# Performance work log

Measured on AMD Instinct MI355X. Metric: run time of the kernel, lower is better.

The kernel has to match this reference:

```python
import jax, jax.numpy as jnp
import numpy as np

B, T, D = 256, 256, 128   # batch, timesteps, latent_dims
U1 = 512                  # units for gru1/gru2
U3 = 64                   # n_output for gru3


def _glorot(key, shape):
    fan_in, fan_out = shape[0], shape[1]
    lim = np.sqrt(6.0 / (fan_in + fan_out))
    return jax.random.uniform(key, shape, jnp.float32, -lim, lim)


def setup_inputs() -> dict:
    key = jax.random.key(0)
    ks = jax.random.split(key, 10)
    inp = {"x": jax.random.normal(ks[0], (B, T, D), jnp.float32)}
    # Keras GRU (reset_after=True): kernel [in, 3u], recurrent_kernel [u, 3u], bias [2, 3u]
    inp["W1"] = _glorot(ks[1], (D, 3 * U1))
    inp["R1"] = _glorot(ks[2], (U1, 3 * U1))
    inp["b1"] = jnp.zeros((2, 3 * U1), jnp.float32)
    inp["W2"] = _glorot(ks[3], (U1, 3 * U1))
    inp["R2"] = _glorot(ks[4], (U1, 3 * U1))
    inp["b2"] = jnp.zeros((2, 3 * U1), jnp.float32)
    inp["W3"] = _glorot(ks[5], (U1, 3 * U3))
    inp["R3"] = _glorot(ks[6], (U3, 3 * U3))
    inp["b3"] = jnp.zeros((2, 3 * U3), jnp.float32)
    return inp


def gru_layer(x, W, R, b, act):
    """Keras GRU, reset_after=True, recurrent_activation=sigmoid, gate order z,r,h.
    x: [B,T,Din] -> [B,T,u] (return_sequences=True)."""
    u = R.shape[0]
    # precompute input projection for all timesteps: [B,T,3u]
    xproj = jnp.einsum('btd,dk->btk', x, W) + b[0]

    def step(h, xt):
        rec = h @ R + b[1]                      # [B,3u]
        xz, xr, xh = jnp.split(xt, 3, axis=-1)
        rz, rr, rh = jnp.split(rec, 3, axis=-1)
        z = jax.nn.sigmoid(xz + rz)
        r = jax.nn.sigmoid(xr + rr)
        hh = act(xh + r * rh)                   # reset gate applied after recurrent matmul
        h_new = z * h + (1.0 - z) * hh
        return h_new, h_new

    h0 = jnp.zeros((x.shape[0], u), x.dtype)
    _, ys = jax.lax.scan(step, h0, jnp.swapaxes(xproj, 0, 1))  # scan over time
    return jnp.swapaxes(ys, 0, 1)


def reference(x, W1, R1, b1, W2, R2, b2, W3, R3, b3):
    h = gru_layer(x, W1, R1, b1, jax.nn.relu)
    h = gru_layer(h, W2, R2, b2, jax.nn.relu)   # dropout skipped (training=False)
    return gru_layer(h, W3, R3, b3, jax.nn.sigmoid)
```

## Files before the change

### kernel.cpp

```cpp
#include <hip/hip_runtime.h>

typedef unsigned short ushort_t;
typedef unsigned int uint_t;
typedef unsigned long long ull_t;
typedef __attribute__((ext_vector_type(8))) short short8;
typedef __attribute__((ext_vector_type(4))) float f32x4;

#define MFMA16(a, b, c) __builtin_amdgcn_mfma_f32_16x16x32_bf16((a), (b), (c), 0, 0, 0)

__device__ __forceinline__ ushort_t f2bf(float f) {
  union { float f; uint_t u; } v; v.f = f;
  uint_t r = v.u + 0x7fffu + ((v.u >> 16) & 1u);
  return (ushort_t)(r >> 16);
}
__device__ __forceinline__ float sigm(float x) { return 1.f / (1.f + __expf(-x)); }

__device__ __forceinline__ short8 ldc(const ushort_t* p) {
  union { ull_t q[2]; short8 v; } u;
  u.q[0] = __hip_atomic_load((const ull_t*)p, __ATOMIC_RELAXED, __HIP_MEMORY_SCOPE_AGENT);
  u.q[1] = __hip_atomic_load((const ull_t*)(p + 4), __ATOMIC_RELAXED, __HIP_MEMORY_SCOPE_AGENT);
  return u.v;
}
template <bool SEQ>
__device__ __forceinline__ short8 ldh(const ushort_t* p) {
  if constexpr (SEQ) return *(const short8*)p;
  else return ldc(p);
}
__device__ __forceinline__ void stc8(ushort_t* p, ull_t v) {
  __hip_atomic_store((ull_t*)p, v, __ATOMIC_RELAXED, __HIP_MEMORY_SCOPE_AGENT);
}
__device__ __forceinline__ void stc4(uint_t* p, uint_t v) {
  __hip_atomic_store(p, v, __ATOMIC_RELAXED, __HIP_MEMORY_SCOPE_AGENT);
}

__device__ __forceinline__ void barrier_l() {
  asm volatile("s_waitcnt lgkmcnt(0)" ::: "memory");
  __builtin_amdgcn_s_barrier();
  asm volatile("" ::: "memory");
}

__device__ __forceinline__ size_t hidx(int ko, int b0, int l15) {
  return (size_t)((ko >> 4) * 256 + b0 + l15) * 16 + (ko & 15);
}

#define OFF_XBF  0UL
#define OFF_W1T  16777216UL
#define OFF_R1T  17170432UL
#define OFF_W2T  18743296UL
#define OFF_R2T  20316160UL
#define OFF_W3T  21889024UL
#define OFF_R3T  22085632UL
#define OFF_CNT  22110208UL
#define OFF_H    22114304UL
#define H1_BYTES_SEQ  (257UL * 262144UL)
#define H3_BYTES_SEQ  (257UL * 32768UL)
#define SEQ_NEED (OFF_H + 2UL * H1_BYTES_SEQ + H3_BYTES_SEQ)
#define H1_BYTES_RING (4UL * 262144UL)

__global__ void k_cvtx(const float* __restrict__ x, ushort_t* __restrict__ xb) {
  const int i = blockIdx.x * 256 + threadIdx.x;
  const int d4 = i & 31;
  const int t = (i >> 5) & 255;
  const int b = i >> 13;
  const float4 v = ((const float4*)x)[i];
  ushort4 o;
  o.x = f2bf(v.x); o.y = f2bf(v.y); o.z = f2bf(v.z); o.w = f2bf(v.w);
  ((ushort4*)xb)[(((t << 8) + b) << 5) + d4] = o;
}

__global__ void k_tr(const float* __restrict__ src, ushort_t* __restrict__ dst,
                     int K, int G, int n) {
  const int i = blockIdx.x * 256 + threadIdx.x;
  if (i >= n) return;
  const int g = i / K, k = i - g * K;
  dst[i] = f2bf(src[(size_t)k * G + g]);
}

__global__ void k_zero(uint_t* h1, uint_t* h2, uint_t* h3, uint_t* cnt) {
  const int i = blockIdx.x * 256 + threadIdx.x;
  if (i < 65536) h1[i] = 0;
  else if (i < 131072) h2[i - 65536] = 0;
  else if (i < 139264) h3[i - 131072] = 0;
  else if (i < 139776) cnt[i - 139264] = 0;
}

template <bool SEQ>
__global__ __launch_bounds__(256, 1)
void gru_main(const ushort_t* __restrict__ xbf,
              const ushort_t* __restrict__ W1t, const ushort_t* __restrict__ R1t,
              const ushort_t* __restrict__ W2t, const ushort_t* __restrict__ R2t,
              const ushort_t* __restrict__ W3t, const ushort_t* __restrict__ R3t,
              const float* __restrict__ b1, const float* __restrict__ b2,
              const float* __restrict__ b3,
              ushort_t* __restrict__ h1s, ushort_t* __restrict__ h2s,
              ushort_t* __restrict__ h3s,
              uint_t* __restrict__ cnt, float* __restrict__ out) {
  __shared__ char ldsb[64512] __attribute__((aligned(16)));
  char* w2b = ldsb + 15360;
#define RGN(r) (*(f32x4*)(ldsb + ((r) << 10) + ((size_t)lane << 4)))
  const int tid = threadIdx.x, bid = blockIdx.x;
  const int grp = bid & 7;
  const int w = bid >> 3;
  const int b0A = grp << 5, b0B = b0A + 16;
  const int lane = tid & 63, wid = tid >> 6;
  const int l15 = lane & 15, quad = lane >> 4, q8 = quad << 3;
  const int lay = wid >> 1, sub = wid & 1;
  const bool isC = (w >= 28);
  const int u = (w << 4) + l15;
  const int u3 = ((w - 28) << 4) + l15;

  if (lay == 1) {
#pragma unroll
    for (int g = 0; g < 3; ++g)
#pragma unroll
      for (int kk = 0; kk < 8; ++kk) {
        const int k2 = sub * 8 + kk;
        const short8 v = *(const short8*)&W2t[(size_t)(g * 512 + u) * 512 + k2 * 32 + q8];
        const int off = ((((g * 16 + l15) << 10) + ((k2 * 32 + q8) << 1)) ^ ((l15 & 7) << 4));
        *(short8*)(w2b + off) = v;
      }
  }

  short8 wreg[33];
  if (lay == 0) {
    if (sub == 0) {
#pragma unroll
      for (int g = 0; g < 3; ++g) {
#pragma unroll
        for (int kk = 0; kk < 4; ++kk)
          wreg[g * 4 + kk] = *(const short8*)&W1t[(size_t)(g * 512 + u) * 128 + kk * 32 + q8];
#pragma unroll
        for (int kk = 0; kk < 5; ++kk)
          wreg[12 + g * 5 + kk] = *(const short8*)&R1t[(size_t)(g * 512 + u) * 512 + kk * 32 + q8];
      }
    } else {
#pragma unroll
      for (int g = 0; g < 3; ++g)
#pragma unroll
        for (int kk = 0; kk < 11; ++kk)
          wreg[g * 11 + kk] = *(const short8*)&R1t[(size_t)(g * 512 + u) * 512 + (5 + kk) * 32 + q8];
    }
  } else {
#pragma unroll
    for (int g = 0; g < 3; ++g)
#pragma unroll
      for (int kk = 0; kk < 8; ++kk)
        wreg[g * 8 + kk] = *(const short8*)&R2t[(size_t)(g * 512 + u) * 512 + (sub * 8 + kk) * 32 + q8];
  }
  __syncthreads();

  const float bzs1 = b1[u] + b1[1536 + u];
  const float brs1 = b1[512 + u] + b1[2048 + u];
  const float bh10 = b1[1024 + u], bh11 = b1[2560 + u];
  const float bzs2 = b2[u] + b2[1536 + u];
  const float brs2 = b2[512 + u] + b2[2048 + u];
  const float bh20 = b2[1024 + u], bh21 = b2[2560 + u];
  float czs = 0, crs = 0, ch0 = 0, ch1 = 0;
  if (isC) {
    czs = b3[u3] + b3[192 + u3];
    crs = b3[64 + u3] + b3[256 + u3];
    ch0 = b3[128 + u3]; ch1 = b3[320 + u3];
  }

  float h1st[4] = {0, 0, 0, 0};
  float h2st[4] = {0, 0, 0, 0};
  float h3st[4] = {0, 0, 0, 0};
  const f32x4 z4 = {0.f, 0.f, 0.f, 0.f};
  uint_t* flags = cnt;

#pragma unroll 1
  for (int s = 0; s < 258; ++s) {
    {
      const uint_t* fl = flags + grp * 32 + (lane & 31);
      while (true) {
        const uint_t v = __hip_atomic_load(fl, __ATOMIC_RELAXED, __HIP_MEMORY_SCOPE_AGENT);
        if (__all((int)(v >= (uint_t)s))) break;
        __builtin_amdgcn_s_sleep(1);
      }
      asm volatile("" ::: "memory");
    }
    const size_t sl_h1rd = (size_t)(SEQ ? s : (s & 3)) * 131072;
    const size_t sl_h1wr = (size_t)(SEQ ? (s + 1) : ((s + 1) & 3)) * 131072;
    const size_t sl_h2rd = (size_t)(SEQ ? (s - 1) : ((s - 1) & 3)) * 131072;
    const size_t sl_h2wr = (size_t)(SEQ ? s : (s & 3)) * 131072;
    const size_t sl_h3rd = (size_t)(SEQ ? (s - 2) : ((s - 2) & 3)) * 16384;
    const size_t sl_h3wr = (size_t)(SEQ ? (s - 1) : ((s - 1) & 3)) * 16384;

    f32x4 azA = z4, arrA = z4, ahxA = z4, ahrA = z4;
    f32x4 azB = z4, arrB = z4, ahxB = z4, ahrB = z4;
    f32x4 dzA = z4, drrA = z4, dhxA = z4, dhrA = z4;
    f32x4 dzB = z4, drrB = z4, dhxB = z4, dhrB = z4;

    if (lay == 0) {
      const ushort_t* h1rd = h1s + sl_h1rd;
      const ushort_t* h2rd = h2s + sl_h2rd;
      if (sub == 0) {
        short8 sx[4], sh[5], s2A[8], s3[2];
        if (s < 256) {
          const ushort_t* xrA = xbf + ((size_t)s * 256 + b0A + l15) * 128;
#pragma unroll
          for (int kk = 0; kk < 4; ++kk) sx[kk] = *(const short8*)&xrA[kk * 32 + q8];
#pragma unroll
          for (int kk = 0; kk < 5; ++kk)
            sh[kk] = ldh<SEQ>(&h1rd[hidx(kk * 32 + q8, b0A, l15)]);
        }
        if (isC && s >= 2) {
          const ushort_t* h3rd = h3s + sl_h3rd;
#pragma unroll
          for (int kk = 0; kk < 8; ++kk)
            s2A[kk] = ldh<SEQ>(&h2rd[hidx(kk * 32 + q8, b0A, l15)]);
#pragma unroll
          for (int kk = 0; kk < 2; ++kk)
            s3[kk] = ldh<SEQ>(&h3rd[hidx(kk * 32 + q8, b0A, l15)]);
        }
        if (s < 256) {
#pragma unroll
          for (int kk = 0; kk < 4; ++kk) {
            azA  = MFMA16(sx[kk], wreg[kk], azA);
            arrA = MFMA16(sx[kk], wreg[4 + kk], arrA);
            ahxA = MFMA16(sx[kk], wreg[8 + kk], ahxA);
          }
#pragma unroll
          for (int kk = 0; kk < 5; ++kk) {
            azA  = MFMA16(sh[kk], wreg[12 + kk], azA);
            arrA = MFMA16(sh[kk], wreg[17 + kk], arrA);
            ahrA = MFMA16(sh[kk], wreg[22 + kk], ahrA);
          }
          const ushort_t* xrB = xbf + ((size_t)s * 256 + b0B + l15) * 128;
#pragma unroll
          for (int kk = 0; kk < 4; ++kk) sx[kk] = *(const short8*)&xrB[kk * 32 + q8];
#pragma unroll
          for (int kk = 0; kk < 5; ++kk)
            sh[kk] = ldh<SEQ>(&h1rd[hidx(kk * 32 + q8, b0B, l15)]);
#pragma unroll
          for (int kk = 0; kk < 4; ++kk) {
            azB  = MFMA16(sx[kk], wreg[kk], azB);
            arrB = MFMA16(sx[kk], wreg[4 + kk], arrB);
            ahxB = MFMA16(sx[kk], wreg[8 + kk], ahxB);
          }
#pragma unroll
          for (int kk = 0; kk < 5; ++kk) {
            azB  = MFMA16(sh[kk], wreg[12 + kk], azB);
            arrB = MFMA16(sh[kk], wreg[17 + kk], arrB);
            ahrB = MFMA16(sh[kk], wreg[22 + kk], ahrB);
          }
        }
        if (isC && s >= 2) {
          const ushort_t* h3rd = h3s + sl_h3rd;
#pragma unroll
          for (int kk = 0; kk < 8; ++kk) {
            const int ko = kk * 32 + q8;
            dzA  = MFMA16(s2A[kk], *(const short8*)&W3t[(size_t)u3 * 512 + ko], dzA);
            drrA = MFMA16(s2A[kk], *(const short8*)&W3t[(size_t)(64 + u3) * 512 + ko], drrA);
            dhxA = MFMA16(s2A[kk], *(const short8*)&W3t[(size_t)(128 + u3) * 512 + ko], dhxA);
          }
#pragma unroll
          for (int kk = 0; kk < 2; ++kk) {
            const int ko = kk * 32 + q8;
            dzA  = MFMA16(s3[kk], *(const short8*)&R3t[(size_t)u3 * 64 + ko], dzA);
            drrA = MFMA16(s3[kk], *(const short8*)&R3t[(size_t)(64 + u3) * 64 + ko], drrA);
            dhrA = MFMA16(s3[kk], *(const short8*)&R3t[(size_t)(128 + u3) * 64 + ko], dhrA);
          }
#pragma unroll
          for (int kk = 0; kk < 8; ++kk)
            s2A[kk] = ldh<SEQ>(&h2rd[hidx(kk * 32 + q8, b0B, l15)]);
#pragma unroll
          for (int kk = 0; kk < 2; ++kk)
            s3[kk] = ldh<SEQ>(&h3rd[hidx(kk * 32 + q8, b0B, l15)]);
#pragma unroll
          for (int kk = 0; kk < 8; ++kk) {
            const int ko = kk * 32 + q8;
            dzB  = MFMA16(s2A[kk], *(const short8*)&W3t[(size_t)u3 * 512 + ko], dzB);
            drrB = MFMA16(s2A[kk], *(const short8*)&W3t[(size_t)(64 + u3) * 512 + ko], drrB);
            dhxB = MFMA16(s2A[kk], *(const short8*)&W3t[(size_t)(128 + u3) * 512 + ko], dhxB);
          }
#pragma unroll
          for (int kk = 0; kk < 2; ++kk) {
            const int ko = kk * 32 + q8;
            dzB  = MFMA16(s3[kk], *(const short8*)&R3t[(size_t)u3 * 64 + ko], dzB);
            drrB = MFMA16(s3[kk], *(const short8*)&R3t[(size_t)(64 + u3) * 64 + ko], drrB);
            dhrB = MFMA16(s3[kk], *(const short8*)&R3t[(size_t)(128 + u3) * 64 + ko], dhrB);
          }
        }
      } else {
        short8 sh[11], s2A[8];
        if (s < 256) {
#pragma unroll
          for (int kk = 0; kk < 11; ++kk)
            sh[kk] = ldh<SEQ>(&h1rd[hidx((5 + kk) * 32 + q8, b0A, l15)]);
        }
        if (isC && s >= 2) {
#pragma unroll
          for (int kk = 0; kk < 8; ++kk)
            s2A[kk] = ldh<SEQ>(&h2rd[hidx((8 + kk) * 32 + q8, b0A, l15)]);
        }
        if (s < 256) {
#pragma unroll
          for (int kk = 0; kk < 11; ++kk) {
            azA  = MFMA16(sh[kk], wreg[kk], azA);
            arrA = MFMA16(sh[kk], wreg[11 + kk], arrA);
            ahrA = MFMA16(sh[kk], wreg[22 + kk], ahrA);
          }
#pragma unroll
          for (int kk = 0; kk < 11; ++kk)
            sh[kk] = ldh<SEQ>(&h1rd[hidx((5 + kk) * 32 + q8, b0B, l15)]);
#pragma unroll
          for (int kk = 0; kk < 11; ++kk) {
            azB  = MFMA16(sh[kk], wreg[kk], azB);
            arrB = MFMA16(sh[kk], wreg[11 + kk], arrB);
            ahrB = MFMA16(sh[kk], wreg[22 + kk], ahrB);
          }
        }
        if (isC && s >= 2) {
#pragma unroll
          for (int kk = 0; kk < 8; ++kk) {
            const int ko = (8 + kk) * 32 + q8;
            dzA  = MFMA16(s2A[kk], *(const short8*)&W3t[(size_t)u3 * 512 + ko], dzA);
            drrA = MFMA16(s2A[kk], *(const short8*)&W3t[(size_t)(64 + u3) * 512 + ko], drrA);
            dhxA = MFMA16(s2A[kk], *(const short8*)&W3t[(size_t)(128 + u3) * 512 + ko], dhxA);
          }
#pragma unroll
          for (int kk = 0; kk < 8; ++kk)
            s2A[kk] = ldh<SEQ>(&h2rd[hidx((8 + kk) * 32 + q8, b0B, l15)]);
#pragma unroll
          for (int kk = 0; kk < 8; ++kk) {
            const int ko = (8 + kk) * 32 + q8;
            dzB  = MFMA16(s2A[kk], *(const short8*)&W3t[(size_t)u3 * 512 + ko], dzB);
            drrB = MFMA16(s2A[kk], *(const short8*)&W3t[(size_t)(64 + u3) * 512 + ko], drrB);
            dhxB = MFMA16(s2A[kk], *(const short8*)&W3t[(size_t)(128 + u3) * 512 + ko], dhxB);
          }
        }
      }
    } else {
      if (s >= 1 && s < 257) {
        const ushort_t* h1rd = h1s + sl_h1rd;
        const ushort_t* h2rd = h2s + sl_h2rd;
        short8 sa[8], sb[8];
#pragma unroll
        for (int kk = 0; kk < 8; ++kk) {
          const size_t ao = hidx((sub * 8 + kk) * 32 + q8, b0A, l15);
          sa[kk] = ldh<SEQ>(&h1rd[ao]);
          sb[kk] = ldh<SEQ>(&h2rd[ao]);
        }
#pragma unroll
        for (int kk = 0; kk < 8; ++kk) {
          const int ko = (sub * 8 + kk) * 32 + q8;
          const int o0 = ((((0 * 16 + l15) << 10) + (ko << 1)) ^ ((l15 & 7) << 4));
          const int o1 = ((((1 * 16 + l15) << 10) + (ko << 1)) ^ ((l15 & 7) << 4));
          const int o2 = ((((2 * 16 + l15) << 10) + (ko << 1)) ^ ((l15 & 7) << 4));
          azA  = MFMA16(sa[kk], *(const short8*)(w2b + o0), azA);
          arrA = MFMA16(sa[kk], *(const short8*)(w2b + o1), arrA);
          ahxA = MFMA16(sa[kk], *(const short8*)(w2b + o2), ahxA);
          azA  = MFMA16(sb[kk], wreg[kk], azA);
          arrA = MFMA16(sb[kk], wreg[8 + kk], arrA);
          ahrA = MFMA16(sb[kk], wreg[16 + kk], ahrA);
        }
#pragma unroll
        for (int kk = 0; kk < 8; ++kk) {
          const size_t ao = hidx((sub * 8 + kk) * 32 + q8, b0B, l15);
          sa[kk] = ldh<SEQ>(&h1rd[ao]);
          sb[kk] = ldh<SEQ>(&h2rd[ao]);
        }
#pragma unroll
        for (int kk = 0; kk < 8; ++kk) {
          const int ko = (sub * 8 + kk) * 32 + q8;
          const int o0 = ((((0 * 16 + l15) << 10) + (ko << 1)) ^ ((l15 & 7) << 4));
          const int o1 = ((((1 * 16 + l15) << 10) + (ko << 1)) ^ ((l15 & 7) << 4));
          const int o2 = ((((2 * 16 + l15) << 10) + (ko << 1)) ^ ((l15 & 7) << 4));
          azB  = MFMA16(sa[kk], *(const short8*)(w2b + o0), azB);
          arrB = MFMA16(sa[kk], *(const short8*)(w2b + o1), arrB);
          ahxB = MFMA16(sa[kk], *(const short8*)(w2b + o2), ahxB);
          azB  = MFMA16(sb[kk], wreg[kk], azB);
          arrB = MFMA16(sb[kk], wreg[8 + kk], arrB);
          ahrB = MFMA16(sb[kk], wreg[16 + kk], ahrB);
        }
      }
    }

    if (lay == 0) {
      if (sub == 1) {
        if (s < 256) { RGN(0) = azA; RGN(1) = arrA; RGN(2) = ahrA; }
      } else {
        if (s < 256) { RGN(3) = azB; RGN(4) = arrB; RGN(5) = ahxB; RGN(6) = ahrB; }
      }
    } else {
      if (s >= 1 && s < 257) {
        if (sub == 1) { RGN(7) = azA; RGN(8) = arrA; RGN(9) = ahxA; RGN(10) = ahrA; }
        else          { RGN(11) = azB; RGN(12) = arrB; RGN(13) = ahxB; RGN(14) = ahrB; }
      }
    }
    barrier_l();

    if (lay == 0) {
      if (sub == 0) {
        if (s < 256) {
          const f32x4 ez = RGN(0), er = RGN(1), ehr = RGN(2);
          ushort_t* stg = (ushort_t*)ldsb;
#pragma unroll
          for (int r = 0; r < 4; ++r) {
            const float z = sigm(azA[r] + ez[r] + bzs1);
            const float rg = sigm(arrA[r] + er[r] + brs1);
            const float hh = fmaxf(ahxA[r] + bh10 + rg * (ahrA[r] + ehr[r] + bh11), 0.f);
            const float hn = z * h1st[r] + (1.f - z) * hh;
            h1st[r] = hn;
            stg[(quad * 4 + r) * 16 + l15] = f2bf(hn);
          }
          asm volatile("s_waitcnt lgkmcnt(0)" ::: "memory");
          stc8(&h1s[sl_h1wr + (size_t)w * 4096 + (size_t)b0A * 16 + lane * 4],
               *(const ull_t*)&stg[lane * 4]);
        }
      } else {
        if (s < 256) {
          const f32x4 ez = RGN(3), er = RGN(4), ehx = RGN(5), ehr = RGN(6);
          ushort_t* stg = (ushort_t*)(ldsb + 3072);
#pragma unroll
          for (int r = 0; r < 4; ++r) {
            const float z = sigm(azB[r] + ez[r] + bzs1);
            const float rg = sigm(arrB[r] + er[r] + brs1);
            const float hh = fmaxf(ehx[r] + bh10 + rg * (ahrB[r] + ehr[r] + bh11), 0.f);
            const float hn = z * h1st[r] + (1.f - z) * hh;
            h1st[r] = hn;
            stg[(quad * 4 + r) * 16 + l15] = f2bf(hn);
          }
          asm volatile("s_waitcnt lgkmcnt(0)" ::: "memory");
          stc8(&h1s[sl_h1wr + (size_t)w * 4096 + (size_t)b0B * 16 + lane * 4],
               *(const ull_t*)&stg[lane * 4]);
        }
      }
    } else {
      if (s >= 1 && s < 257) {
        if (sub == 0) {
          const f32x4 ez = RGN(7), er = RGN(8), ehx = RGN(9), ehr = RGN(10);
          ushort_t* stg = (ushort_t*)(ldsb + 7168);
#pragma unroll
          for (int r = 0; r < 4; ++r) {
            const float z = sigm(azA[r] + ez[r] + bzs2);
            const float rg = sigm(arrA[r] + er[r] + brs2);
            const float hh = fmaxf(ahxA[r] + ehx[r] + bh20 + rg * (ahrA[r] + ehr[r] + bh21), 0.f);
            const float hn = z * h2st[r] + (1.f - z) * hh;
            h2st[r] = hn;
            stg[(quad * 4 + r) * 16 + l15] = f2bf(hn);
          }
          asm volatile("s_waitcnt lgkmcnt(0)" ::: "memory");
          stc8(&h2s[sl_h2wr + (size_t)w * 4096 + (size_t)b0A * 16 + lane * 4],
               *(const ull_t*)&stg[lane * 4]);
        } else {
          const f32x4 ez = RGN(11), er = RGN(12), ehx = RGN(13), ehr = RGN(14);
          ushort_t* stg = (ushort_t*)(ldsb + 11264);
#pragma unroll
          for (int r = 0; r < 4; ++r) {
            const float z = sigm(azB[r] + ez[r] + bzs2);
            const float rg = sigm(arrB[r] + er[r] + brs2);
            const float hh = fmaxf(ahxB[r] + ehx[r] + bh20 + rg * (ahrB[r] + ehr[r] + bh21), 0.f);
            const float hn = z * h2st[r] + (1.f - z) * hh;
            h2st[r] = hn;
            stg[(quad * 4 + r) * 16 + l15] = f2bf(hn);
          }
          asm volatile("s_waitcnt lgkmcnt(0)" ::: "memory");
          stc8(&h2s[sl_h2wr + (size_t)w * 4096 + (size_t)b0B * 16 + lane * 4],
               *(const ull_t*)&stg[lane * 4]);
        }
      }
    }
    barrier_l();

    if (isC && lay == 0 && s >= 2) {
      if (sub == 1) { RGN(0) = dzA; RGN(1) = drrA; RGN(2) = dhxA; }
      else          { RGN(3) = dzB; RGN(4) = drrB; RGN(5) = dhxB; RGN(6) = dhrB; }
    }
    barrier_l();
    if (isC && lay == 0 && s >= 2) {
      const int t3 = s - 2;
      if (sub == 0) {
        const f32x4 ez = RGN(0), er = RGN(1), ehx = RGN(2);
        ushort_t* stg = (ushort_t*)ldsb;
#pragma unroll
        for (int r = 0; r < 4; ++r) {
          const float z = sigm(dzA[r] + ez[r] + czs);
          const float rg = sigm(drrA[r] + er[r] + crs);
          const float hh = sigm(dhxA[r] + ehx[r] + ch0 + rg * (dhrA[r] + ch1));
          const float hn = z * h3st[r] + (1.f - z) * hh;
          h3st[r] = hn;
          out[((size_t)(b0A + quad * 4 + r) * 256 + t3) * 64 + u3] = hn;
          stg[(quad * 4 + r) * 16 + l15] = f2bf(hn);
        }
        asm volatile("s_waitcnt lgkmcnt(0)" ::: "memory");
        stc8(&h3s[sl_h3wr + (size_t)(w - 28) * 4096 + (size_t)b0A * 16 + lane * 4],
             *(const ull_t*)&stg[lane * 4]);
      } else {
        const f32x4 ez = RGN(3), er = RGN(4), ehx = RGN(5), edhr = RGN(6);
        ushort_t* stg = (ushort_t*)(ldsb + 3072);
#pragma unroll
        for (int r = 0; r < 4; ++r) {
          const float z = sigm(dzB[r] + ez[r] + czs);
          const float rg = sigm(drrB[r] + er[r] + crs);
          const float hh = sigm(dhxB[r] + ehx[r] + ch0 + rg * (edhr[r] + ch1));
          const float hn = z * h3st[r] + (1.f - z) * hh;
          h3st[r] = hn;
          out[((size_t)(b0B + quad * 4 + r) * 256 + t3) * 64 + u3] = hn;
          stg[(quad * 4 + r) * 16 + l15] = f2bf(hn);
        }
        asm volatile("s_waitcnt lgkmcnt(0)" ::: "memory");
        stc8(&h3s[sl_h3wr + (size_t)(w - 28) * 4096 + (size_t)b0B * 16 + lane * 4],
             *(const ull_t*)&stg[lane * 4]);
      }
    }
    __syncthreads();
    if (tid == 0) stc4(&flags[grp * 32 + w], (uint_t)(s + 1));
  }
#undef RGN
}

extern "C" void kernel_launch(void* const* d_in, const int* in_sizes, int n_in,
                              void* d_out, int out_size, void* d_ws, size_t ws_size,
                              hipStream_t stream) {
  const float* x  = (const float*)d_in[0];
  const float* W1 = (const float*)d_in[1];
  const float* R1 = (const float*)d_in[2];
  const float* b1 = (const float*)d_in[3];
  const float* W2 = (const float*)d_in[4];
  const float* R2 = (const float*)d_in[5];
  const float* b2 = (const float*)d_in[6];
  const float* W3 = (const float*)d_in[7];
  const float* R3 = (const float*)d_in[8];
  const float* b3 = (const float*)d_in[9];
  char* ws = (char*)d_ws;
  ushort_t* xbf = (ushort_t*)(ws + OFF_XBF);
  ushort_t* W1t = (ushort_t*)(ws + OFF_W1T);
  ushort_t* R1t = (ushort_t*)(ws + OFF_R1T);
  ushort_t* W2t = (ushort_t*)(ws + OFF_W2T);
  ushort_t* R2t = (ushort_t*)(ws + OFF_R2T);
  ushort_t* W3t = (ushort_t*)(ws + OFF_W3T);
  ushort_t* R3t = (ushort_t*)(ws + OFF_R3T);
  uint_t* cntp  = (uint_t*)(ws + OFF_CNT);

  const bool seq = (ws_size >= SEQ_NEED);
  ushort_t *h1p, *h2p, *h3p;
  if (seq) {
    h1p = (ushort_t*)(ws + OFF_H);
    h2p = (ushort_t*)(ws + OFF_H + H1_BYTES_SEQ);
    h3p = (ushort_t*)(ws + OFF_H + 2UL * H1_BYTES_SEQ);
  } else {
    h1p = (ushort_t*)(ws + OFF_H);
    h2p = (ushort_t*)(ws + OFF_H + H1_BYTES_RING);
    h3p = (ushort_t*)(ws + OFF_H + 2UL * H1_BYTES_RING);
  }

  k_cvtx<<<8192, 256, 0, stream>>>(x, xbf);
  k_tr<<<768, 256, 0, stream>>>(W1, W1t, 128, 1536, 196608);
  k_tr<<<3072, 256, 0, stream>>>(R1, R1t, 512, 1536, 786432);
  k_tr<<<3072, 256, 0, stream>>>(W2, W2t, 512, 1536, 786432);
  k_tr<<<3072, 256, 0, stream>>>(R2, R2t, 512, 1536, 786432);
  k_tr<<<384, 256, 0, stream>>>(W3, W3t, 512, 192, 98304);
  k_tr<<<48, 256, 0, stream>>>(R3, R3t, 64, 192, 12288);
  k_zero<<<546, 256, 0, stream>>>((uint_t*)h1p, (uint_t*)h2p, (uint_t*)h3p, cntp);
  if (seq) {
    gru_main<true><<<256, 256, 0, stream>>>(xbf, W1t, R1t, W2t, R2t, W3t, R3t,
                                            b1, b2, b3, h1p, h2p, h3p, cntp,
                                            (float*)d_out);
  } else {
    gru_main<false><<<256, 256, 0, stream>>>(xbf, W1t, R1t, W2t, R2t, W3t, R3t,
                                             b1, b2, b3, h1p, h2p, h3p, cntp,
                                             (float*)d_out);
  }
}
```

Baseline: 2.428 ms.

## Move layer-3 input projection onto layer-2 waves that already load h2

Layer 3's input projection (h2 times W3) used to be computed by the layer-0 waves, which loaded h2 separately. It now runs on the layer-1 waves, which already hold the h2 fragments in registers for their own recurrent matmul, so they reuse them. Only the small recurrent h3 matmul stays on the layer-0 waves. The partial sums are combined through LDS before the gate math, which removes duplicate h2 loads and evens out MFMA work between the two wave groups. In exchange, the layer-1 waves now run extra iterations (doL3 while doL2 is false), and the reduction moves more accumulators through LDS.

```diff
diff --git a/kernel.cpp b/kernel.cpp
--- a/kernel.cpp
+++ b/kernel.cpp
@@ -188,14 +188,14 @@
 
     f32x4 azA = z4, arrA = z4, ahxA = z4, ahrA = z4;
     f32x4 azB = z4, arrB = z4, ahxB = z4, ahrB = z4;
-    f32x4 dzA = z4, drrA = z4, dhxA = z4, dhrA = z4;
-    f32x4 dzB = z4, drrB = z4, dhxB = z4, dhrB = z4;
+    f32x4 l3zA = z4, l3rA = z4, l3hA = z4;
+    f32x4 l3zB = z4, l3rB = z4, l3hB = z4;
+    const bool doL3 = isC && (s >= 2);
 
     if (lay == 0) {
       const ushort_t* h1rd = h1s + sl_h1rd;
-      const ushort_t* h2rd = h2s + sl_h2rd;
       if (sub == 0) {
-        short8 sx[4], sh[5], s2A[8], s3[2];
+        short8 sx[4], sh[5], s3A[2], s3B[2];
         if (s < 256) {
           const ushort_t* xrA = xbf + ((size_t)s * 256 + b0A + l15) * 128;
 #pragma unroll
@@ -204,14 +204,13 @@
           for (int kk = 0; kk < 5; ++kk)
             sh[kk] = ldh<SEQ>(&h1rd[hidx(kk * 32 + q8, b0A, l15)]);
         }
-        if (isC && s >= 2) {
+        if (doL3) {
           const ushort_t* h3rd = h3s + sl_h3rd;
 #pragma unroll
-          for (int kk = 0; kk < 8; ++kk)
-            s2A[kk] = ldh<SEQ>(&h2rd[hidx(kk * 32 + q8, b0A, l15)]);
-#pragma unroll
-          for (int kk = 0; kk < 2; ++kk)
-            s3[kk] = ldh<SEQ>(&h3rd[hidx(kk * 32 + q8, b0A, l15)]);
+          for (int kk = 0; kk < 2; ++kk) {
+            s3A[kk] = ldh<SEQ>(&h3rd[hidx(kk * 32 + q8, b0A, l15)]);
+            s3B[kk] = ldh<SEQ>(&h3rd[hidx(kk * 32 + q8, b0B, l15)]);
+          }
         }
         if (s < 256) {
 #pragma unroll
@@ -232,6 +231,23 @@
 #pragma unroll
           for (int kk = 0; kk < 5; ++kk)
             sh[kk] = ldh<SEQ>(&h1rd[hidx(kk * 32 + q8, b0B, l15)]);
+        }
+        if (doL3) {
+#pragma unroll
+          for (int kk = 0; kk < 2; ++kk) {
+            const int ko = kk * 32 + q8;
+            const short8 rz = *(const short8*)&R3t[(size_t)u3 * 64 + ko];
+            const short8 rr = *(const short8*)&R3t[(size_t)(64 + u3) * 64 + ko];
+            const short8 rh = *(const short8*)&R3t[(size_t)(128 + u3) * 64 + ko];
+            l3zA = MFMA16(s3A[kk], rz, l3zA);
+            l3rA = MFMA16(s3A[kk], rr, l3rA);
+            l3hA = MFMA16(s3A[kk], rh, l3hA);
+            l3zB = MFMA16(s3B[kk], rz, l3zB);
+            l3rB = MFMA16(s3B[kk], rr, l3rB);
+            l3hB = MFMA16(s3B[kk], rh, l3hB);
+          }
+        }
+        if (s < 256) {
 #pragma unroll
           for (int kk = 0; kk < 4; ++kk) {
             azB  = MFMA16(sx[kk], wreg[kk], azB);
@@ -245,56 +261,12 @@
             ahrB = MFMA16(sh[kk], wreg[22 + kk], ahrB);
           }
         }
-        if (isC && s >= 2) {
-          const ushort_t* h3rd = h3s + sl_h3rd;
-#pragma unroll
-          for (int kk = 0; kk < 8; ++kk) {
-            const int ko = kk * 32 + q8;
-            dzA  = MFMA16(s2A[kk], *(const short8*)&W3t[(size_t)u3 * 512 + ko], dzA);
-            drrA = MFMA16(s2A[kk], *(const short8*)&W3t[(size_t)(64 + u3) * 512 + ko], drrA);
-            dhxA = MFMA16(s2A[kk], *(const short8*)&W3t[(size_t)(128 + u3) * 512 + ko], dhxA);
-          }
-#pragma unroll
-          for (int kk = 0; kk < 2; ++kk) {
-            const int ko = kk * 32 + q8;
-            dzA  = MFMA16(s3[kk], *(const short8*)&R3t[(size_t)u3 * 64 + ko], dzA);
-            drrA = MFMA16(s3[kk], *(const short8*)&R3t[(size_t)(64 + u3) * 64 + ko], drrA);
-            dhrA = MFMA16(s3[kk], *(const short8*)&R3t[(size_t)(128 + u3) * 64 + ko], dhrA);
-          }
-#pragma unroll
-          for (int kk = 0; kk < 8; ++kk)
-            s2A[kk] = ldh<SEQ>(&h2rd[hidx(kk * 32 + q8, b0B, l15)]);
-#pragma unroll
-          for (int kk = 0; kk < 2; ++kk)
-            s3[kk] = ldh<SEQ>(&h3rd[hidx(kk * 32 + q8, b0B, l15)]);
-#pragma unroll
-          for (int kk = 0; kk < 8; ++kk) {
-            const int ko = kk * 32 + q8;
-            dzB  = MFMA16(s2A[kk], *(const short8*)&W3t[(size_t)u3 * 512 + ko], dzB);
-            drrB = MFMA16(s2A[kk], *(const short8*)&W3t[(size_t)(64 + u3) * 512 + ko], drrB);
-            dhxB = MFMA16(s2A[kk], *(const short8*)&W3t[(size_t)(128 + u3) * 512 + ko], dhxB);
-          }
-#pragma unroll
-          for (int kk = 0; kk < 2; ++kk) {
-            const int ko = kk * 32 + q8;
-            dzB  = MFMA16(s3[kk], *(const short8*)&R3t[(size_t)u3 * 64 + ko], dzB);
-            drrB = MFMA16(s3[kk], *(const short8*)&R3t[(size_t)(64 + u3) * 64 + ko], drrB);
-            dhrB = MFMA16(s3[kk], *(const short8*)&R3t[(size_t)(128 + u3) * 64 + ko], dhrB);
-          }
-        }
       } else {
-        short8 sh[11], s2A[8];
         if (s < 256) {
+          short8 sh[11];
 #pragma unroll
           for (int kk = 0; kk < 11; ++kk)
             sh[kk] = ldh<SEQ>(&h1rd[hidx((5 + kk) * 32 + q8, b0A, l15)]);
-        }
-        if (isC && s >= 2) {
-#pragma unroll
-          for (int kk = 0; kk < 8; ++kk)
-            s2A[kk] = ldh<SEQ>(&h2rd[hidx((8 + kk) * 32 + q8, b0A, l15)]);
-        }
-        if (s < 256) {
 #pragma unroll
           for (int kk = 0; kk < 11; ++kk) {
             azA  = MFMA16(sh[kk], wreg[kk], azA);
@@ -311,68 +283,66 @@
             ahrB = MFMA16(sh[kk], wreg[22 + kk], ahrB);
           }
         }
-        if (isC && s >= 2) {
-#pragma unroll
-          for (int kk = 0; kk < 8; ++kk) {
-            const int ko = (8 + kk) * 32 + q8;
-            dzA  = MFMA16(s2A[kk], *(const short8*)&W3t[(size_t)u3 * 512 + ko], dzA);
-            drrA = MFMA16(s2A[kk], *(const short8*)&W3t[(size_t)(64 + u3) * 512 + ko], drrA);
-            dhxA = MFMA16(s2A[kk], *(const short8*)&W3t[(size_t)(128 + u3) * 512 + ko], dhxA);
-          }
-#pragma unroll
-          for (int kk = 0; kk < 8; ++kk)
-            s2A[kk] = ldh<SEQ>(&h2rd[hidx((8 + kk) * 32 + q8, b0B, l15)]);
-#pragma unroll
-          for (int kk = 0; kk < 8; ++kk) {
-            const int ko = (8 + kk) * 32 + q8;
-            dzB  = MFMA16(s2A[kk], *(const short8*)&W3t[(size_t)u3 * 512 + ko], dzB);
-            drrB = MFMA16(s2A[kk], *(const short8*)&W3t[(size_t)(64 + u3) * 512 + ko], drrB);
-            dhxB = MFMA16(s2A[kk], *(const short8*)&W3t[(size_t)(128 + u3) * 512 + ko], dhxB);
-          }
-        }
       }
     } else {
-      if (s >= 1 && s < 257) {
+      const bool doL2 = (s >= 1 && s < 257);
+      if (doL2 || doL3) {
         const ushort_t* h1rd = h1s + sl_h1rd;
         const ushort_t* h2rd = h2s + sl_h2rd;
         short8 sa[8], sb[8];
-#pragma unroll
-        for (int kk = 0; kk < 8; ++kk) {
-          const size_t ao = hidx((sub * 8 + kk) * 32 + q8, b0A, l15);
-          sa[kk] = ldh<SEQ>(&h1rd[ao]);
-          sb[kk] = ldh<SEQ>(&h2rd[ao]);
-        }
+        if (doL2)
+#pragma unroll
+          for (int kk = 0; kk < 8; ++kk)
+            sa[kk] = ldh<SEQ>(&h1rd[hidx((sub * 8 + kk) * 32 + q8, b0A, l15)]);
+#pragma unroll
+        for (int kk = 0; kk < 8; ++kk)
+          sb[kk] = ldh<SEQ>(&h2rd[hidx((sub * 8 + kk) * 32 + q8, b0A, l15)]);
 #pragma unroll
         for (int kk = 0; kk < 8; ++kk) {
           const int ko = (sub * 8 + kk) * 32 + q8;
-          const int o0 = ((((0 * 16 + l15) << 10) + (ko << 1)) ^ ((l15 & 7) << 4));
-          const int o1 = ((((1 * 16 + l15) << 10) + (ko << 1)) ^ ((l15 & 7) << 4));
-          const int o2 = ((((2 * 16 + l15) << 10) + (ko << 1)) ^ ((l15 & 7) << 4));
-          azA  = MFMA16(sa[kk], *(const short8*)(w2b + o0), azA);
-          arrA = MFMA16(sa[kk], *(const short8*)(w2b + o1), arrA);
-          ahxA = MFMA16(sa[kk], *(const short8*)(w2b + o2), ahxA);
-          azA  = MFMA16(sb[kk], wreg[kk], azA);
-          arrA = MFMA16(sb[kk], wreg[8 + kk], arrA);
-          ahrA = MFMA16(sb[kk], wreg[16 + kk], ahrA);
-        }
-#pragma unroll
-        for (int kk = 0; kk < 8; ++kk) {
-          const size_t ao = hidx((sub * 8 + kk) * 32 + q8, b0B, l15);
-          sa[kk] = ldh<SEQ>(&h1rd[ao]);
-          sb[kk] = ldh<SEQ>(&h2rd[ao]);
-        }
+          if (doL2) {
+            const int o0 = ((((0 * 16 + l15) << 10) + (ko << 1)) ^ ((l15 & 7) << 4));
+            const int o1 = ((((1 * 16 + l15) << 10) + (ko << 1)) ^ ((l15 & 7) << 4));
+            const int o2 = ((((2 * 16 + l15) << 10) + (ko << 1)) ^ ((l15 & 7) << 4));
+            azA  = MFMA16(sa[kk], *(const short8*)(w2b + o0), azA);
+            arrA = MFMA16(sa[kk], *(const short8*)(w2b + o1), arrA);
+            ahxA = MFMA16(sa[kk], *(const short8*)(w2b + o2), ahxA);
+            azA  = MFMA16(sb[kk], wreg[kk], azA);
+            arrA = MFMA16(sb[kk], wreg[8 + kk], arrA);
+            ahrA = MFMA16(sb[kk], wreg[16 + kk], ahrA);
+          }
+          if (doL3) {
+            l3zA = MFMA16(sb[kk], *(const short8*)&W3t[(size_t)u3 * 512 + ko], l3zA);
+            l3rA = MFMA16(sb[kk], *(const short8*)&W3t[(size_t)(64 + u3) * 512 + ko], l3rA);
+            l3hA = MFMA16(sb[kk], *(const short8*)&W3t[(size_t)(128 + u3) * 512 + ko], l3hA);
+          }
+        }
+        if (doL2)
+#pragma unroll
+          for (int kk = 0; kk < 8; ++kk)
+            sa[kk] = ldh<SEQ>(&h1rd[hidx((sub * 8 + kk) * 32 + q8, b0B, l15)]);
+#pragma unroll
+        for (int kk = 0; kk < 8; ++kk)
+          sb[kk] = ldh<SEQ>(&h2rd[hidx((sub * 8 + kk) * 32 + q8, b0B, l15)]);
 #pragma unroll
         for (int kk = 0; kk < 8; ++kk) {
           const int ko = (sub * 8 + kk) * 32 + q8;
-          const int o0 = ((((0 * 16 + l15) << 10) + (ko << 1)) ^ ((l15 & 7) << 4));
-          const int o1 = ((((1 * 16 + l15) << 10) + (ko << 1)) ^ ((l15 & 7) << 4));
-          const int o2 = ((((2 * 16 + l15) << 10) + (ko << 1)) ^ ((l15 & 7) << 4));
-          azB  = MFMA16(sa[kk], *(const short8*)(w2b + o0), azB);
-          arrB = MFMA16(sa[kk], *(const short8*)(w2b + o1), arrB);
-          ahxB = MFMA16(sa[kk], *(const short8*)(w2b + o2), ahxB);
-          azB  = MFMA16(sb[kk], wreg[kk], azB);
-          arrB = MFMA16(sb[kk], wreg[8 + kk], arrB);
-          ahrB = MFMA16(sb[kk], wreg[16 + kk], ahrB);
+          if (doL2) {
+            const int o0 = ((((0 * 16 + l15) << 10) + (ko << 1)) ^ ((l15 & 7) << 4));
+            const int o1 = ((((1 * 16 + l15) << 10) + (ko << 1)) ^ ((l15 & 7) << 4));
+            const int o2 = ((((2 * 16 + l15) << 10) + (ko << 1)) ^ ((l15 & 7) << 4));
+            azB  = MFMA16(sa[kk], *(const short8*)(w2b + o0), azB);
+            arrB = MFMA16(sa[kk], *(const short8*)(w2b + o1), arrB);
+            ahxB = MFMA16(sa[kk], *(const short8*)(w2b + o2), ahxB);
+            azB  = MFMA16(sb[kk], wreg[kk], azB);
+            arrB = MFMA16(sb[kk], wreg[8 + kk], arrB);
+            ahrB = MFMA16(sb[kk], wreg[16 + kk], ahrB);
+          }
+          if (doL3) {
+            l3zB = MFMA16(sb[kk], *(const short8*)&W3t[(size_t)u3 * 512 + ko], l3zB);
+            l3rB = MFMA16(sb[kk], *(const short8*)&W3t[(size_t)(64 + u3) * 512 + ko], l3rB);
+            l3hB = MFMA16(sb[kk], *(const short8*)&W3t[(size_t)(128 + u3) * 512 + ko], l3hB);
+          }
         }
       }
     }
@@ -462,23 +432,31 @@
         }
       }
     }
-    barrier_l();
-
-    if (isC && lay == 0 && s >= 2) {
-      if (sub == 1) { RGN(0) = dzA; RGN(1) = drrA; RGN(2) = dhxA; }
-      else          { RGN(3) = dzB; RGN(4) = drrB; RGN(5) = dhxB; RGN(6) = dhrB; }
-    }
-    barrier_l();
-    if (isC && lay == 0 && s >= 2) {
+
+    if (doL3) {
+      barrier_l();
+      if (lay == 1) {
+        if (sub == 0) {
+          RGN(0) = l3zA; RGN(1) = l3rA; RGN(2) = l3hA;
+          RGN(3) = l3zB; RGN(4) = l3rB; RGN(5) = l3hB;
+        } else {
+          RGN(6) = l3zA; RGN(7) = l3rA; RGN(8) = l3hA;
+          RGN(9) = l3zB; RGN(10) = l3rB; RGN(11) = l3hB;
+        }
+      } else if (sub == 0) {
+        RGN(12) = l3zB; RGN(13) = l3rB; RGN(14) = l3hB;
+      }
+      barrier_l();
       const int t3 = s - 2;
-      if (sub == 0) {
-        const f32x4 ez = RGN(0), er = RGN(1), ehx = RGN(2);
+      if (lay == 0 && sub == 0) {
+        const f32x4 pz0 = RGN(0), pr0 = RGN(1), px0 = RGN(2);
+        const f32x4 pz1 = RGN(6), pr1 = RGN(7), px1 = RGN(8);
         ushort_t* stg = (ushort_t*)ldsb;
 #pragma unroll
         for (int r = 0; r < 4; ++r) {
-          const float z = sigm(dzA[r] + ez[r] + czs);
-          const float rg = sigm(drrA[r] + er[r] + crs);
-          const float hh = sigm(dhxA[r] + ehx[r] + ch0 + rg * (dhrA[r] + ch1));
+          const float z = sigm(l3zA[r] + pz0[r] + pz1[r] + czs);
+          const float rg = sigm(l3rA[r] + pr0[r] + pr1[r] + crs);
+          const float hh = sigm(px0[r] + px1[r] + ch0 + rg * (l3hA[r] + ch1));
           const float hn = z * h3st[r] + (1.f - z) * hh;
           h3st[r] = hn;
           out[((size_t)(b0A + quad * 4 + r) * 256 + t3) * 64 + u3] = hn;
@@ -487,14 +465,17 @@
         asm volatile("s_waitcnt lgkmcnt(0)" ::: "memory");
         stc8(&h3s[sl_h3wr + (size_t)(w - 28) * 4096 + (size_t)b0A * 16 + lane * 4],
              *(const ull_t*)&stg[lane * 4]);
-      } else {
-        const f32x4 ez = RGN(3), er = RGN(4), ehx = RGN(5), edhr = RGN(6);
+      }
+      if (lay == 0 && sub == 1) {
+        const f32x4 rz = RGN(12), rr = RGN(13), rh = RGN(14);
+        const f32x4 pz0 = RGN(3), pr0 = RGN(4), px0 = RGN(5);
+        const f32x4 pz1 = RGN(9), pr1 = RGN(10), px1 = RGN(11);
         ushort_t* stg = (ushort_t*)(ldsb + 3072);
 #pragma unroll
         for (int r = 0; r < 4; ++r) {
-          const float z = sigm(dzB[r] + ez[r] + czs);
-          const float rg = sigm(drrB[r] + er[r] + crs);
-          const float hh = sigm(dhxB[r] + ehx[r] + ch0 + rg * (edhr[r] + ch1));
+          const float z = sigm(rz[r] + pz0[r] + pz1[r] + czs);
+          const float rg = sigm(rr[r] + pr0[r] + pr1[r] + crs);
+          const float hh = sigm(px0[r] + px1[r] + ch0 + rg * (rh[r] + ch1));
           const float hn = z * h3st[r] + (1.f - z) * hh;
           h3st[r] = hn;
           out[((size_t)(b0B + quad * 4 + r) * 256 + t3) * 64 + u3] = hn;
```

New measurement: 2.831 ms. 1.17x slower.
